# Kernel optimization log

Hardware: AMD Instinct MI355X
Metric: run time of the kernel (lower is better)

Reference implementation:

```python
import jax, jax.numpy as jnp
import numpy as np

N_EMBD = 448
HEAD_SIZE = 64

def setup_inputs() -> dict:
    key = jax.random.key(0)
    k1, k2, k3, k4 = jax.random.split(key, 4)
    B, T = 16, 2048
    x = jax.random.normal(k1, (B, T, N_EMBD), dtype=jnp.float32)
    # nn.Linear(n_embd, head_size, bias=False): weight shape (head_size, n_embd); y = x @ W.T
    s = 1.0 / np.sqrt(N_EMBD)
    Wk = jax.random.uniform(k2, (HEAD_SIZE, N_EMBD), jnp.float32, -s, s)
    Wq = jax.random.uniform(k3, (HEAD_SIZE, N_EMBD), jnp.float32, -s, s)
    Wv = jax.random.uniform(k4, (HEAD_SIZE, N_EMBD), jnp.float32, -s, s)
    return {"x": x, "Wk": Wk, "Wq": Wq, "Wv": Wv}

def reference(x, Wk, Wq, Wv):
    B, T, C = x.shape
    k = jnp.einsum('btc,hc->bth', x, Wk)  # (B,T,H)
    q = jnp.einsum('btc,hc->bth', x, Wq)
    v = jnp.einsum('btc,hc->bth', x, Wv)
    scale = 1.0 / jnp.sqrt(jnp.float32(C))  # NOTE: scales by sqrt(n_embd), as in source
    wei = jnp.einsum('bth,bsh->bts', q, k) * scale  # (B,T,T)
    causal = jnp.tril(jnp.ones((T, T), dtype=bool))
    wei = jnp.where(causal[None, :, :], wei, -jnp.inf)
    wei = jax.nn.softmax(wei, axis=-1)
    # dropout is identity in eval mode
    out = jnp.einsum('bts,bsh->bth', wei, v)  # (B,T,H)
    return out
```

## Files before the change

### kernel.cpp

```cpp
#include <hip/hip_runtime.h>
#include <math.h>

#define BT 32768
#define NC 448
#define NH 64
#define TT 2048

typedef __bf16 bf16x8 __attribute__((ext_vector_type(8)));
typedef float  f32x4  __attribute__((ext_vector_type(4)));

__device__ __forceinline__ unsigned short f2bf(float f) {
  unsigned u = __builtin_bit_cast(unsigned, f);
  return (unsigned short)((u + 0x7FFFu + ((u >> 16) & 1u)) >> 16);
}
__device__ __forceinline__ ushort4 f2bf4(float4 v) {
  ushort4 b; b.x = f2bf(v.x); b.y = f2bf(v.y); b.z = f2bf(v.z); b.w = f2bf(v.w);
  return b;
}
__device__ __forceinline__ float bf2f(unsigned short u) {
  return __builtin_bit_cast(float, (unsigned)u << 16);
}


__global__ __launch_bounds__(256) void wprep_kernel(
    const float* __restrict__ Wk, const float* __restrict__ Wq,
    const float* __restrict__ Wv, unsigned short* __restrict__ wp)
{
  int idx = blockIdx.x * 256 + threadIdx.x;
  int r = idx & 63;
  int t = idx >> 6;
  int g = t & 7; t >>= 3;
  int ch = t % 7, p = t / 7;
  const float* W = (p == 0) ? Wk : ((p == 1) ? Wq : Wv);
  const float* src = &W[(size_t)r * NC + ch * 64 + g * 8];
  float4 a = *(const float4*)src;
  float4 b = *(const float4*)(src + 4);
  *(ushort4*)&wp[(size_t)idx * 8]     = f2bf4(a);
  *(ushort4*)&wp[(size_t)idx * 8 + 4] = f2bf4(b);
}

__global__ __launch_bounds__(256) void proj_kernel(
    const float* __restrict__ x, const unsigned short* __restrict__ wp,
    unsigned short* __restrict__ kws, unsigned short* __restrict__ qws,
    unsigned short* __restrict__ vws)
{
  __shared__ unsigned short xs[2][4096];
  const int tid = threadIdx.x;
  const int w = tid >> 6, lane = tid & 63;
  const int q = lane >> 4, l15 = lane & 15;
  const int r0 = blockIdx.x * 64;

  f32x4 acc[3][4];
#pragma unroll
  for (int p = 0; p < 3; ++p)
#pragma unroll
    for (int t = 0; t < 4; ++t) acc[p][t] = f32x4{0.f, 0.f, 0.f, 0.f};

  const int c0 = (tid & 15) * 4, r_ = tid >> 4;
  const int wbase = (w * 16 + l15) * 8;

  float4 xr[4];
  bf16x8 wfr[3][2], wnx[3][2];
#pragma unroll
  for (int i = 0; i < 4; ++i)
    xr[i] = *(const float4*)&x[(size_t)(r0 + r_ + 16 * i) * NC + c0];
#pragma unroll
  for (int p = 0; p < 3; ++p)
#pragma unroll
    for (int ks = 0; ks < 2; ++ks)
      wfr[p][ks] = *(const bf16x8*)&wp[(size_t)((p * 7 + 0) * 8 + (q + 4 * ks)) * 512 + wbase];

  for (int ch = 0; ch < 7; ++ch) {
    const int cur = ch & 1;
#pragma unroll
    for (int i = 0; i < 4; ++i) {
      int r = r_ + 16 * i;
      int off = r * 64 + (((c0 >> 3) ^ (r & 7)) << 3) + (c0 & 7);
      *(ushort4*)&xs[cur][off] = f2bf4(xr[i]);
    }
    __syncthreads();
    if (ch < 6) {
      int kc = (ch + 1) * 64;
#pragma unroll
      for (int i = 0; i < 4; ++i)
        xr[i] = *(const float4*)&x[(size_t)(r0 + r_ + 16 * i) * NC + kc + c0];
#pragma unroll
      for (int p = 0; p < 3; ++p)
#pragma unroll
        for (int ks = 0; ks < 2; ++ks)
          wnx[p][ks] = *(const bf16x8*)&wp[(size_t)((p * 7 + ch + 1) * 8 + (q + 4 * ks)) * 512 + wbase];
    }
#pragma unroll
    for (int ks = 0; ks < 2; ++ks) {
#pragma unroll
      for (int t = 0; t < 4; ++t) {
        int xrow = t * 16 + l15;
        bf16x8 xf = *(const bf16x8*)&xs[cur][xrow * 64 + (((q + 4 * ks) ^ (xrow & 7)) << 3)];
        acc[0][t] = __builtin_amdgcn_mfma_f32_16x16x32_bf16(wfr[0][ks], xf, acc[0][t], 0, 0, 0);
        acc[1][t] = __builtin_amdgcn_mfma_f32_16x16x32_bf16(xf, wfr[1][ks], acc[1][t], 0, 0, 0);
        acc[2][t] = __builtin_amdgcn_mfma_f32_16x16x32_bf16(xf, wfr[2][ks], acc[2][t], 0, 0, 0);
      }
    }
    if (ch < 6) {
#pragma unroll
      for (int p = 0; p < 3; ++p)
#pragma unroll
        for (int ks = 0; ks < 2; ++ks)
          wfr[p][ks] = wnx[p][ks];
    }
  }

  const size_t tile = (size_t)blockIdx.x * 4096;
#pragma unroll
  for (int t = 0; t < 4; ++t) {
    int j = t * 16 + l15;
    ushort4 bb; bb.x = f2bf(acc[0][t][0]); bb.y = f2bf(acc[0][t][1]);
    bb.z = f2bf(acc[0][t][2]); bb.w = f2bf(acc[0][t][3]);
    *(ushort4*)&kws[tile + j * 64 + (((2 * w + (q >> 1)) ^ (j & 7)) << 3) + ((q & 1) << 2)] = bb;
  }
  {
    const float qs = 0.068161075f;
    int h = w * 16 + l15;
#pragma unroll
    for (int t = 0; t < 4; ++t)
#pragma unroll
      for (int rr = 0; rr < 4; ++rr) {
        int R = r0 + t * 16 + q * 4 + rr;
        qws[(size_t)R * 64 + h] = f2bf(acc[1][t][rr] * qs);
      }
  }
  {
    int h = w * 16 + l15;
#pragma unroll
    for (int t = 0; t < 4; ++t) {
      ushort4 bb; bb.x = f2bf(acc[2][t][0]); bb.y = f2bf(acc[2][t][1]);
      bb.z = f2bf(acc[2][t][2]); bb.w = f2bf(acc[2][t][3]);
      *(ushort4*)&vws[tile + h * 64 + (((2 * t + (q >> 1)) ^ (h & 7)) << 3) + ((q & 1) << 2)] = bb;
    }
  }
}

__global__ __launch_bounds__(256) void attn_partial(
    const unsigned short* __restrict__ kws, const unsigned short* __restrict__ qws,
    const unsigned short* __restrict__ vws, float* __restrict__ out,
    unsigned short* __restrict__ opart, float* __restrict__ mlpart)
{
  __shared__ unsigned short ksm[2][4096];
  __shared__ unsigned short vtm[2][4096];
  __shared__ unsigned short psm[4096];
  const int bx = blockIdx.x, b = blockIdx.y;
  int qt, kt0, ktn, ci; bool direct;
  if (bx < 16)      { qt = 16 + bx; kt0 = 0;  ktn = 16;     ci = 0; direct = false; }
  else if (bx < 32) { qt = 47 - bx; kt0 = 16; ktn = qt + 1; ci = 1; direct = false; }
  else              { qt = 47 - bx; kt0 = 0;  ktn = qt + 1; ci = 0; direct = true;  }
  const int nt = ktn - kt0;

  const int tid = threadIdx.x;
  const int w = tid >> 6, lane = tid & 63;
  const int q = lane >> 4, l15 = lane & 15;
  const int t0 = b * TT + qt * 64;
  const int l7 = l15 & 7;

  bf16x8 qf[2];
#pragma unroll
  for (int ks = 0; ks < 2; ++ks)
    qf[ks] = *(const bf16x8*)&qws[(size_t)(t0 + w * 16 + l15) * 64 + 32 * ks + q * 8];

  f32x4 oacc[4];
#pragma unroll
  for (int ht = 0; ht < 4; ++ht) oacc[ht] = f32x4{0.f, 0.f, 0.f, 0.f};
  float m_i = -INFINITY, l_i = 0.f;

  uint4 kr0, kr1, vr0, vr1;
  {
    const unsigned short* kt_ = kws + (size_t)(b * 32 + kt0) * 4096;
    const unsigned short* vt_ = vws + (size_t)(b * 32 + kt0) * 4096;
    kr0 = *(const uint4*)&kt_[tid * 8];  kr1 = *(const uint4*)&kt_[2048 + tid * 8];
    vr0 = *(const uint4*)&vt_[tid * 8];  vr1 = *(const uint4*)&vt_[2048 + tid * 8];
  }

  for (int it = 0; it < nt; ++it) {
    const int kt = kt0 + it;
    const int cur = it & 1;
    *(uint4*)&ksm[cur][tid * 8] = kr0;  *(uint4*)&ksm[cur][2048 + tid * 8] = kr1;
    *(uint4*)&vtm[cur][tid * 8] = vr0;  *(uint4*)&vtm[cur][2048 + tid * 8] = vr1;
    __syncthreads();
    if (it + 1 < nt) {
      const unsigned short* kt_ = kws + (size_t)(b * 32 + kt + 1) * 4096;
      const unsigned short* vt_ = vws + (size_t)(b * 32 + kt + 1) * 4096;
      kr0 = *(const uint4*)&kt_[tid * 8];  kr1 = *(const uint4*)&kt_[2048 + tid * 8];
      vr0 = *(const uint4*)&vt_[tid * 8];  vr1 = *(const uint4*)&vt_[2048 + tid * 8];
    }

    f32x4 sacc[4];
#pragma unroll
    for (int jt = 0; jt < 4; ++jt) sacc[jt] = f32x4{0.f, 0.f, 0.f, 0.f};
#pragma unroll
    for (int jt = 0; jt < 4; ++jt) {
      int j = jt * 16 + l15;
#pragma unroll
      for (int ks = 0; ks < 2; ++ks) {
        bf16x8 kf = *(const bf16x8*)&ksm[cur][j * 64 + (((q + 4 * ks) ^ (j & 7)) << 3)];
        sacc[jt] = __builtin_amdgcn_mfma_f32_16x16x32_bf16(kf, qf[ks], sacc[jt], 0, 0, 0);
      }
    }

    if (kt == qt) {
      int iloc = w * 16 + l15;
#pragma unroll
      for (int jt = 0; jt < 4; ++jt)
#pragma unroll
        for (int rr = 0; rr < 4; ++rr)
          if (jt * 16 + q * 4 + rr > iloc) sacc[jt][rr] = -INFINITY;
    }

    float mx = -INFINITY;
#pragma unroll
    for (int jt = 0; jt < 4; ++jt)
#pragma unroll
      for (int rr = 0; rr < 4; ++rr) mx = fmaxf(mx, sacc[jt][rr]);
    mx = fmaxf(mx, __shfl_xor(mx, 16));
    mx = fmaxf(mx, __shfl_xor(mx, 32));
    float mn = fmaxf(m_i, mx);
    float alpha = exp2f(m_i - mn);
    m_i = mn;
    float p[4][4], rs = 0.f;
#pragma unroll
    for (int jt = 0; jt < 4; ++jt)
#pragma unroll
      for (int rr = 0; rr < 4; ++rr) {
        float pv = exp2f(sacc[jt][rr] - mn);
        p[jt][rr] = pv; rs += pv;
      }
    rs += __shfl_xor(rs, 16);
    rs += __shfl_xor(rs, 32);
    l_i = l_i * alpha + rs;

    float a_t[4];
#pragma unroll
    for (int rr = 0; rr < 4; ++rr) a_t[rr] = __shfl(alpha, q * 4 + rr);
#pragma unroll
    for (int ht = 0; ht < 4; ++ht)
#pragma unroll
      for (int rr = 0; rr < 4; ++rr) oacc[ht][rr] *= a_t[rr];

    {
      int row = w * 16 + l15;
#pragma unroll
      for (int jt = 0; jt < 4; ++jt) {
        ushort4 bb; bb.x = f2bf(p[jt][0]); bb.y = f2bf(p[jt][1]);
        bb.z = f2bf(p[jt][2]); bb.w = f2bf(p[jt][3]);
        *(ushort4*)&psm[row * 64 + (((2 * jt + (q >> 1)) ^ l7) << 3) + ((q & 1) << 2)] = bb;
      }
    }

#pragma unroll
    for (int ks2 = 0; ks2 < 2; ++ks2) {
      int prow = w * 16 + l15;
      bf16x8 pf = *(const bf16x8*)&psm[prow * 64 + (((q + 4 * ks2) ^ l7) << 3)];
#pragma unroll
      for (int ht = 0; ht < 4; ++ht) {
        int h = ht * 16 + l15;
        bf16x8 vf = *(const bf16x8*)&vtm[cur][h * 64 + (((q + 4 * ks2) ^ l7) << 3)];
        oacc[ht] = __builtin_amdgcn_mfma_f32_16x16x32_bf16(pf, vf, oacc[ht], 0, 0, 0);
      }
    }
  }

  if (direct) {
    float l_t[4];
#pragma unroll
    for (int rr = 0; rr < 4; ++rr) l_t[rr] = __shfl(l_i, q * 4 + rr);
#pragma unroll
    for (int rr = 0; rr < 4; ++rr) {
      float inv = 1.f / l_t[rr];
      int R = t0 + w * 16 + q * 4 + rr;
#pragma unroll
      for (int ht = 0; ht < 4; ++ht)
        out[(size_t)R * 64 + ht * 16 + l15] = oacc[ht][rr] * inv;
    }
  } else {
    const size_t slot = (size_t)(b * 16 + (qt - 16)) * 2 + ci;
    unsigned short* Op = opart + slot * 4096;
#pragma unroll
    for (int rr = 0; rr < 4; ++rr) {
      int rloc = w * 16 + q * 4 + rr;
#pragma unroll
      for (int ht = 0; ht < 4; ++ht)
        Op[rloc * 64 + ht * 16 + l15] = f2bf(oacc[ht][rr]);
    }
    if (q == 0) {
      mlpart[slot * 128 + w * 16 + l15]      = m_i;
      mlpart[slot * 128 + 64 + w * 16 + l15] = l_i;
    }
  }
}

__global__ __launch_bounds__(256) void combine_kernel(
    const unsigned short* __restrict__ opart, const float* __restrict__ mlpart,
    float* __restrict__ out)
{
  const int qtc = blockIdx.x, b = blockIdx.y;
  const int qt = 16 + qtc;
  const int t = threadIdx.x;
  const int r = t >> 2, c0 = (t & 3) * 16;
  const size_t s0 = (size_t)(b * 16 + qtc) * 2;

  float m0 = mlpart[s0 * 128 + r],       l0 = mlpart[s0 * 128 + 64 + r];
  float m1 = mlpart[(s0 + 1) * 128 + r], l1 = mlpart[(s0 + 1) * 128 + 64 + r];
  float m  = fmaxf(m0, m1);
  float w0 = exp2f(m0 - m), w1 = exp2f(m1 - m);
  float inv = 1.f / (w0 * l0 + w1 * l1);
  w0 *= inv; w1 *= inv;

  const unsigned short* O0 = opart + s0 * 4096 + r * 64 + c0;
  const unsigned short* O1 = opart + (s0 + 1) * 4096 + r * 64 + c0;
  union { uint4 v; unsigned short e[8]; } a0, a1;
  float* op = out + (size_t)(b * TT + qt * 64 + r) * 64;
#pragma unroll
  for (int half = 0; half < 2; ++half) {
    a0.v = *(const uint4*)&O0[half * 8];
    a1.v = *(const uint4*)&O1[half * 8];
    float res[8];
#pragma unroll
    for (int u = 0; u < 8; ++u)
      res[u] = w0 * bf2f(a0.e[u]) + w1 * bf2f(a1.e[u]);
    *(float4*)&op[c0 + half * 8]     = make_float4(res[0], res[1], res[2], res[3]);
    *(float4*)&op[c0 + half * 8 + 4] = make_float4(res[4], res[5], res[6], res[7]);
  }
}

extern "C" void kernel_launch(void* const* d_in, const int* in_sizes, int n_in,
                              void* d_out, int out_size, void* d_ws, size_t ws_size,
                              hipStream_t stream) {
  const float* x  = (const float*)d_in[0];
  const float* Wk = (const float*)d_in[1];
  const float* Wq = (const float*)d_in[2];
  const float* Wv = (const float*)d_in[3];
  unsigned short* kws = (unsigned short*)d_ws;
  unsigned short* qws = kws + (size_t)BT * NH;
  unsigned short* vws = qws + (size_t)BT * NH;
  unsigned short* opart = vws + (size_t)BT * NH;
  float* mlpart = (float*)(opart + (size_t)512 * 4096);
  float* out = (float*)d_out;
  unsigned short* wprep = opart;

  wprep_kernel<<<dim3(42), 256, 0, stream>>>(Wk, Wq, Wv, wprep);
  proj_kernel<<<dim3(512), 256, 0, stream>>>(x, wprep, kws, qws, vws);
  attn_partial<<<dim3(48, 16), 256, 0, stream>>>(kws, qws, vws, out, opart, mlpart);
  combine_kernel<<<dim3(16, 16), 256, 0, stream>>>(opart, mlpart, out);
}
```

Measured before the change: 142.1 us.

## Split attention into 8-tile KV chunks, keep P in registers, add lazy rescale

Work is now split into chunks of at most 8 key tiles per block, so the grid grows from 48 to 80 blocks per batch and load is spread more evenly. The combine kernel is generalised to merge a variable number of partials. The P matrix is moved into the MFMA operand layout with cross-lane shuffles instead of a round trip through shared memory. The online-softmax rescale is skipped unless the running max grows by more than a threshold, and s_setprio is raised around the MFMA sections. Native bf16 conversion replaces the manual rounding. The risks are more partial-output traffic, more combine work, and the lazy-rescale threshold affecting numerical range.

```diff
diff --git a/kernel.cpp b/kernel.cpp
--- a/kernel.cpp
+++ b/kernel.cpp
@@ -7,11 +7,12 @@
 #define TT 2048
 
 typedef __bf16 bf16x8 __attribute__((ext_vector_type(8)));
+typedef __bf16 bf16x2 __attribute__((ext_vector_type(2)));
 typedef float  f32x4  __attribute__((ext_vector_type(4)));
 
 __device__ __forceinline__ unsigned short f2bf(float f) {
-  unsigned u = __builtin_bit_cast(unsigned, f);
-  return (unsigned short)((u + 0x7FFFu + ((u >> 16) & 1u)) >> 16);
+  __bf16 h = (__bf16)f;
+  return __builtin_bit_cast(unsigned short, h);
 }
 __device__ __forceinline__ ushort4 f2bf4(float4 v) {
   ushort4 b; b.x = f2bf(v.x); b.y = f2bf(v.y); b.z = f2bf(v.z); b.w = f2bf(v.w);
@@ -147,19 +148,35 @@
 {
   __shared__ unsigned short ksm[2][4096];
   __shared__ unsigned short vtm[2][4096];
-  __shared__ unsigned short psm[4096];
   const int bx = blockIdx.x, b = blockIdx.y;
-  int qt, kt0, ktn, ci; bool direct;
-  if (bx < 16)      { qt = 16 + bx; kt0 = 0;  ktn = 16;     ci = 0; direct = false; }
-  else if (bx < 32) { qt = 47 - bx; kt0 = 16; ktn = qt + 1; ci = 1; direct = false; }
-  else              { qt = 47 - bx; kt0 = 0;  ktn = qt + 1; ci = 0; direct = true;  }
+  int qt = 0, c = 0;
+  {
+    int idx = bx;
+    if (idx < 52) {
+      for (int q2 = 31; q2 >= 7; --q2) {
+        int L = (q2 + 1) >> 3;
+        if (idx < L) { qt = q2; c = idx; break; }
+        idx -= L;
+      }
+    } else {
+      idx -= 52;
+      for (int q2 = 31; q2 >= 0; --q2) {
+        if ((q2 + 1) & 7) {
+          if (idx == 0) { qt = q2; c = (q2 + 1) >> 3; break; }
+          --idx;
+        }
+      }
+    }
+  }
+  const int kt0 = c * 8;
+  const int ktn = min(kt0 + 8, qt + 1);
   const int nt = ktn - kt0;
+  const bool direct = (qt <= 7);
 
   const int tid = threadIdx.x;
   const int w = tid >> 6, lane = tid & 63;
   const int q = lane >> 4, l15 = lane & 15;
   const int t0 = b * TT + qt * 64;
-  const int l7 = l15 & 7;
 
   bf16x8 qf[2];
 #pragma unroll
@@ -178,6 +195,10 @@
     kr0 = *(const uint4*)&kt_[tid * 8];  kr1 = *(const uint4*)&kt_[2048 + tid * 8];
     vr0 = *(const uint4*)&vt_[tid * 8];  vr1 = *(const uint4*)&vt_[2048 + tid * 8];
   }
+
+  const int srcA = (((2 * q) & 3) << 4) + l15;
+  const int srcB = (((2 * q + 1) & 3) << 4) + l15;
+  const bool hiq = (q >> 1) != 0;
 
   for (int it = 0; it < nt; ++it) {
     const int kt = kt0 + it;
@@ -195,6 +216,7 @@
     f32x4 sacc[4];
 #pragma unroll
     for (int jt = 0; jt < 4; ++jt) sacc[jt] = f32x4{0.f, 0.f, 0.f, 0.f};
+    __builtin_amdgcn_s_setprio(1);
 #pragma unroll
     for (int jt = 0; jt < 4; ++jt) {
       int j = jt * 16 + l15;
@@ -204,6 +226,7 @@
         sacc[jt] = __builtin_amdgcn_mfma_f32_16x16x32_bf16(kf, qf[ks], sacc[jt], 0, 0, 0);
       }
     }
+    __builtin_amdgcn_s_setprio(0);
 
     if (kt == qt) {
       int iloc = w * 16 + l15;
@@ -221,50 +244,61 @@
       for (int rr = 0; rr < 4; ++rr) mx = fmaxf(mx, sacc[jt][rr]);
     mx = fmaxf(mx, __shfl_xor(mx, 16));
     mx = fmaxf(mx, __shfl_xor(mx, 32));
-    float mn = fmaxf(m_i, mx);
-    float alpha = exp2f(m_i - mn);
-    m_i = mn;
-    float p[4][4], rs = 0.f;
+    if (!__all(mx <= m_i + 11.0f)) {
+      float mn = fmaxf(m_i, mx);
+      float alpha = exp2f(m_i - mn);
+      m_i = mn;
+      l_i *= alpha;
+      float a_t[4];
+#pragma unroll
+      for (int rr = 0; rr < 4; ++rr) a_t[rr] = __shfl(alpha, q * 4 + rr);
+#pragma unroll
+      for (int ht = 0; ht < 4; ++ht)
+#pragma unroll
+        for (int rr = 0; rr < 4; ++rr) oacc[ht][rr] *= a_t[rr];
+    }
+    float rs = 0.f;
 #pragma unroll
     for (int jt = 0; jt < 4; ++jt)
 #pragma unroll
       for (int rr = 0; rr < 4; ++rr) {
-        float pv = exp2f(sacc[jt][rr] - mn);
-        p[jt][rr] = pv; rs += pv;
+        float pv = exp2f(sacc[jt][rr] - m_i);
+        sacc[jt][rr] = pv; rs += pv;
       }
     rs += __shfl_xor(rs, 16);
     rs += __shfl_xor(rs, 32);
-    l_i = l_i * alpha + rs;
-
-    float a_t[4];
-#pragma unroll
-    for (int rr = 0; rr < 4; ++rr) a_t[rr] = __shfl(alpha, q * 4 + rr);
-#pragma unroll
-    for (int ht = 0; ht < 4; ++ht)
-#pragma unroll
-      for (int rr = 0; rr < 4; ++rr) oacc[ht][rr] *= a_t[rr];
-
-    {
-      int row = w * 16 + l15;
-#pragma unroll
-      for (int jt = 0; jt < 4; ++jt) {
-        ushort4 bb; bb.x = f2bf(p[jt][0]); bb.y = f2bf(p[jt][1]);
-        bb.z = f2bf(p[jt][2]); bb.w = f2bf(p[jt][3]);
-        *(ushort4*)&psm[row * 64 + (((2 * jt + (q >> 1)) ^ l7) << 3) + ((q & 1) << 2)] = bb;
-      }
-    }
-
+    l_i += rs;
+
+    unsigned pku[4][2];
+#pragma unroll
+    for (int jt = 0; jt < 4; ++jt)
+#pragma unroll
+      for (int h2 = 0; h2 < 2; ++h2) {
+        bf16x2 tpk;
+        tpk[0] = (__bf16)sacc[jt][2 * h2];
+        tpk[1] = (__bf16)sacc[jt][2 * h2 + 1];
+        pku[jt][h2] = __builtin_bit_cast(unsigned, tpk);
+      }
+
+    __builtin_amdgcn_s_setprio(1);
 #pragma unroll
     for (int ks2 = 0; ks2 < 2; ++ks2) {
-      int prow = w * 16 + l15;
-      bf16x8 pf = *(const bf16x8*)&psm[prow * 64 + (((q + 4 * ks2) ^ l7) << 3)];
+      unsigned a0 = __shfl(pku[2 * ks2][0], srcA), b0 = __shfl(pku[2 * ks2 + 1][0], srcA);
+      unsigned a1 = __shfl(pku[2 * ks2][1], srcA), b1 = __shfl(pku[2 * ks2 + 1][1], srcA);
+      unsigned a2 = __shfl(pku[2 * ks2][0], srcB), b2 = __shfl(pku[2 * ks2 + 1][0], srcB);
+      unsigned a3 = __shfl(pku[2 * ks2][1], srcB), b3 = __shfl(pku[2 * ks2 + 1][1], srcB);
+      uint4 wds;
+      wds.x = hiq ? b0 : a0; wds.y = hiq ? b1 : a1;
+      wds.z = hiq ? b2 : a2; wds.w = hiq ? b3 : a3;
+      bf16x8 pf = __builtin_bit_cast(bf16x8, wds);
 #pragma unroll
       for (int ht = 0; ht < 4; ++ht) {
         int h = ht * 16 + l15;
-        bf16x8 vf = *(const bf16x8*)&vtm[cur][h * 64 + (((q + 4 * ks2) ^ l7) << 3)];
+        bf16x8 vf = *(const bf16x8*)&vtm[cur][h * 64 + (((q + 4 * ks2) ^ (h & 7)) << 3)];
         oacc[ht] = __builtin_amdgcn_mfma_f32_16x16x32_bf16(pf, vf, oacc[ht], 0, 0, 0);
       }
     }
+    __builtin_amdgcn_s_setprio(0);
   }
 
   if (direct) {
@@ -280,7 +314,8 @@
         out[(size_t)R * 64 + ht * 16 + l15] = oacc[ht][rr] * inv;
     }
   } else {
-    const size_t slot = (size_t)(b * 16 + (qt - 16)) * 2 + ci;
+    const int pre = (qt < 16) ? 2 * (qt - 8) : (qt < 24 ? 16 + 3 * (qt - 16) : 40 + 4 * (qt - 24));
+    const size_t slot = (size_t)b * 72 + pre + c;
     unsigned short* Op = opart + slot * 4096;
 #pragma unroll
     for (int rr = 0; rr < 4; ++rr) {
@@ -301,33 +336,41 @@
     float* __restrict__ out)
 {
   const int qtc = blockIdx.x, b = blockIdx.y;
-  const int qt = 16 + qtc;
+  const int qt = 8 + qtc;
+  const int nc = (qt >> 3) + 1;
+  const int pre = (qt < 16) ? 2 * (qt - 8) : (qt < 24 ? 16 + 3 * (qt - 16) : 40 + 4 * (qt - 24));
+  const size_t s0 = (size_t)b * 72 + pre;
   const int t = threadIdx.x;
   const int r = t >> 2, c0 = (t & 3) * 16;
-  const size_t s0 = (size_t)(b * 16 + qtc) * 2;
-
-  float m0 = mlpart[s0 * 128 + r],       l0 = mlpart[s0 * 128 + 64 + r];
-  float m1 = mlpart[(s0 + 1) * 128 + r], l1 = mlpart[(s0 + 1) * 128 + 64 + r];
-  float m  = fmaxf(m0, m1);
-  float w0 = exp2f(m0 - m), w1 = exp2f(m1 - m);
-  float inv = 1.f / (w0 * l0 + w1 * l1);
-  w0 *= inv; w1 *= inv;
-
-  const unsigned short* O0 = opart + s0 * 4096 + r * 64 + c0;
-  const unsigned short* O1 = opart + (s0 + 1) * 4096 + r * 64 + c0;
-  union { uint4 v; unsigned short e[8]; } a0, a1;
-  float* op = out + (size_t)(b * TT + qt * 64 + r) * 64;
-#pragma unroll
-  for (int half = 0; half < 2; ++half) {
-    a0.v = *(const uint4*)&O0[half * 8];
-    a1.v = *(const uint4*)&O1[half * 8];
-    float res[8];
-#pragma unroll
-    for (int u = 0; u < 8; ++u)
-      res[u] = w0 * bf2f(a0.e[u]) + w1 * bf2f(a1.e[u]);
-    *(float4*)&op[c0 + half * 8]     = make_float4(res[0], res[1], res[2], res[3]);
-    *(float4*)&op[c0 + half * 8 + 4] = make_float4(res[4], res[5], res[6], res[7]);
-  }
+
+  float m = -INFINITY;
+  for (int i = 0; i < nc; ++i)
+    m = fmaxf(m, mlpart[(s0 + i) * 128 + r]);
+  float wsum = 0.f;
+  for (int i = 0; i < nc; ++i)
+    wsum += exp2f(mlpart[(s0 + i) * 128 + r] - m) * mlpart[(s0 + i) * 128 + 64 + r];
+  const float inv = 1.f / wsum;
+
+  float res[16];
+#pragma unroll
+  for (int u = 0; u < 16; ++u) res[u] = 0.f;
+  for (int i = 0; i < nc; ++i) {
+    float wi = exp2f(mlpart[(s0 + i) * 128 + r] - m) * inv;
+    const unsigned short* O = opart + (s0 + i) * 4096 + r * 64 + c0;
+    union { uint4 v; unsigned short e[8]; } u0, u1;
+    u0.v = *(const uint4*)&O[0];
+    u1.v = *(const uint4*)&O[8];
+#pragma unroll
+    for (int u = 0; u < 8; ++u) {
+      res[u]     += wi * bf2f(u0.e[u]);
+      res[8 + u] += wi * bf2f(u1.e[u]);
+    }
+  }
+  float* op = out + (size_t)(b * TT + qt * 64 + r) * 64 + c0;
+  *(float4*)&op[0]  = make_float4(res[0], res[1], res[2], res[3]);
+  *(float4*)&op[4]  = make_float4(res[4], res[5], res[6], res[7]);
+  *(float4*)&op[8]  = make_float4(res[8], res[9], res[10], res[11]);
+  *(float4*)&op[12] = make_float4(res[12], res[13], res[14], res[15]);
 }
 
 extern "C" void kernel_launch(void* const* d_in, const int* in_sizes, int n_in,
@@ -341,12 +384,12 @@
   unsigned short* qws = kws + (size_t)BT * NH;
   unsigned short* vws = qws + (size_t)BT * NH;
   unsigned short* opart = vws + (size_t)BT * NH;
-  float* mlpart = (float*)(opart + (size_t)512 * 4096);
+  float* mlpart = (float*)(opart + (size_t)1152 * 4096);
   float* out = (float*)d_out;
   unsigned short* wprep = opart;
 
   wprep_kernel<<<dim3(42), 256, 0, stream>>>(Wk, Wq, Wv, wprep);
   proj_kernel<<<dim3(512), 256, 0, stream>>>(x, wprep, kws, qws, vws);
-  attn_partial<<<dim3(48, 16), 256, 0, stream>>>(kws, qws, vws, out, opart, mlpart);
-  combine_kernel<<<dim3(16, 16), 256, 0, stream>>>(opart, mlpart, out);
-}
+  attn_partial<<<dim3(80, 16), 256, 0, stream>>>(kws, qws, vws, out, opart, mlpart);
+  combine_kernel<<<dim3(24, 16), 256, 0, stream>>>(opart, mlpart, out);
+}
```

Measured after the change: 141.3 us. Within noise of the previous version (-0.6%).
